# Kernel tuning notes

Measured on AMD Instinct MI355X. Metric: run time of the kernel, lower is better.

Reference implementation:

```python
import jax, jax.numpy as jnp
import numpy as np
from jax import lax

REPR_IN = (32, 16, 8)   # multiplicities of l=0,1,2 fields
SIZE = 5                # cubic kernel size (odd)
PAD = SIZE // 2


def setup_inputs() -> dict:
    key = jax.random.key(0)
    k1, k2 = jax.random.split(key)
    c_in = sum(mul * (2 * l + 1) for l, mul in enumerate(REPR_IN))   # 120
    n_non_scalar = sum(REPR_IN[1:])                                   # 24
    x = jax.random.normal(k1, (2, c_in, 48, 48, 48), dtype=jnp.float32)
    # SE3Convolution materialized as its effective dense conv kernel [O, I, D, H, W]
    fan_in = c_in * SIZE ** 3
    w_gate = jax.random.normal(k2, (n_non_scalar, c_in, SIZE, SIZE, SIZE), dtype=jnp.float32) / np.sqrt(fan_in)
    return {"x": x, "w_gate": w_gate}


def reference(x, w_gate):
    B, _, X, Y, Z = x.shape
    # Gate branch: 3D conv (same padding) -> sigmoid, one scalar gate per non-scalar field
    g = jax.nn.sigmoid(
        lax.conv_general_dilated(
            x, w_gate,
            window_strides=(1, 1, 1),
            padding=[(PAD, PAD)] * 3,
            dimension_numbers=("NCDHW", "OIDHW", "NCDHW"),
        )
    )  # [B, n_non_scalar, X, Y, Z]

    parts = []
    begin_x = 0
    begin_g = 0
    for l, mul in enumerate(REPR_IN):
        if mul == 0:
            continue
        dim = 2 * l + 1
        field_x = x[:, begin_x:begin_x + mul * dim]
        if l == 0:
            # scalar activation on the l=0 block
            parts.append(jax.nn.relu(field_x))
        else:
            # broadcast gate over the 2l+1 components of each field copy
            fx = field_x.reshape(B, mul, dim, X, Y, Z)
            fg = g[:, begin_g:begin_g + mul][:, :, None]      # [B, mul, 1, X, Y, Z]
            begin_g += mul
            parts.append((fx * fg).reshape(B, mul * dim, X, Y, Z))
        begin_x += mul * dim
    return jnp.concatenate(parts, axis=1)
```

## Files before the change

### kernel.cpp

```cpp
#include <hip/hip_runtime.h>

typedef __attribute__((ext_vector_type(8))) short short8;
typedef __attribute__((ext_vector_type(4))) float f32x4;

#define SDIM 48
#define SS   (48*48)
#define SSS  (48*48*48)
#define CIN  120
#define CIP  128
#define NCO  24
#define ZP   52
#define NTAP 125

#define WP_USHORTS (4*25*5*32*32)
#define WP_BYTES   ((size_t)WP_USHORTS*2)
#define XT_USHORTS ((size_t)2*48*48*ZP*CIP)
#define XT_BYTES   (XT_USHORTS*2)
#define WTOT_F32   (NCO*CIN*NTAP)

#define A_CHUNKS 1664
#define ABUF_USH 13312
#define GLP      25

__device__ __forceinline__ unsigned short f2bf(float f){
    unsigned u = __float_as_uint(f);
    u = (u + 0x7FFFu + ((u >> 16) & 1u)) >> 16;
    return (unsigned short)u;
}

__device__ __forceinline__ void gload_lds16(const unsigned short* g, unsigned short* l)
{
    __builtin_amdgcn_global_load_lds(
        (const __attribute__((address_space(1))) unsigned int*)g,
        (__attribute__((address_space(3))) unsigned int*)l,
        16, 0, 0);
}


__global__ __launch_bounds__(256)
void transpose_x(const float* __restrict__ x, unsigned short* __restrict__ xt)
{
    __shared__ unsigned short sm[CIN*50];
    int bid = blockIdx.x;
    const int iy = bid % 48; bid /= 48;
    const int ix = bid % 48;
    const int b  = bid / 48;
    const int tid = threadIdx.x;

    const float* __restrict__ src = x + (size_t)b*CIN*SSS + ((size_t)ix*48 + iy)*48;
    for (int idx = tid; idx < CIN*48; idx += 256) {
        int ci = idx / 48, z = idx - ci*48;
        sm[ci*50 + z] = f2bf(src[(size_t)ci*SSS + z]);
    }
    __syncthreads();
    unsigned short* __restrict__ dst = xt + (((size_t)(b*48 + ix)*48) + iy)*ZP*CIP;
    for (int odx = tid; odx < ZP*CIP; odx += 256) {
        int zp = odx >> 7, ci = odx & 127;
        int z = zp - 2;
        unsigned short v = 0;
        if (ci < CIN && (unsigned)z < 48u) v = sm[ci*50 + z];
        dst[odx] = v;
    }
}

__global__ __launch_bounds__(256)
void repack_w_bf16(const float* __restrict__ w, unsigned short* __restrict__ wp)
{
    int idx = blockIdx.x*256 + threadIdx.x;
    if (idx >= WP_USHORTS) return;
    int cik = idx & 31;
    int co  = (idx >> 5) & 31;
    int dz  = (idx >> 10) % 5;
    int t   = (idx / 5120) % 25;
    int cc  = idx / 128000;
    int ci  = cc*32 + cik;
    float v = 0.f;
    if (co < NCO && ci < CIN)
        v = w[(size_t)(co*CIN + ci)*NTAP + t*5 + dz];
    wp[idx] = f2bf(v);
}

#define MFMA16(a,b,c) __builtin_amdgcn_mfma_f32_16x16x32_bf16(a,b,c,0,0,0)

__global__ __launch_bounds__(128, 3)
void conv_mfma(const unsigned short* __restrict__ xt,
               const unsigned short* __restrict__ wp,
               const float* __restrict__ x,
               float* __restrict__ out)
{
    __shared__ __align__(16) unsigned short As[ABUF_USH];

    int bid = (blockIdx.x & 7) * 144 + (blockIdx.x >> 3);
    const int oyq = bid % 12; bid /= 12;
    const int ox = bid % 48;
    const int b  = bid / 48;

    const int tid = threadIdx.x;
    const int wave = tid >> 6, lane = tid & 63;
    const int l15 = lane & 15, l4 = lane >> 4;
    const int iy0 = oyq*4 - 2;

    const int dxlo = (ox < 2) ? (2 - ox) : 0;
    const int dxhi = (ox > 45) ? (49 - ox) : 4;
    const int ndx  = dxhi - dxlo + 1;

    int goff[13];
    bool ok[13];
#pragma unroll
    for (int k = 0; k < 13; ++k) {
        int L = k*128 + tid;
        int iyl = L / 208, r = L - iyl*208;
        int zp = r >> 2, sf = r & 3;
        int sg = sf ^ ((zp >> 1) & 3);
        int iy = iy0 + iyl;
        ok[k]   = (unsigned)iy < 48u;
        goff[k] = (iy*52 + zp)*128 + sg*8;
    }
    const unsigned short* zsrc = xt + (lane & 31)*8;

    f32x4 acc[2][3][2];
#pragma unroll
    for (int oh = 0; oh < 2; ++oh)
#pragma unroll
      for (int zb = 0; zb < 3; ++zb)
#pragma unroll
        for (int nt = 0; nt < 2; ++nt) acc[oh][zb][nt] = (f32x4){0,0,0,0};

#pragma unroll 1
    for (int cc = 0; cc < 4; ++cc) {
#pragma unroll 1
      for (int dxi = 0; dxi < ndx; ++dxi) {
        const int dx = dxlo + dxi;
        const int ix = ox + dx - 2;
        const unsigned short* __restrict__ slab =
            xt + (size_t)(b*48 + ix)*(48*52*128) + cc*32;

        __syncthreads();
#pragma unroll
        for (int k = 0; k < 13; ++k) {
            const unsigned short* src = ok[k] ? (slab + goff[k]) : zsrc;
            gload_lds16(src, As + k*1024 + wave*512);
        }
        asm volatile("s_waitcnt vmcnt(0)" ::: "memory");
        __builtin_amdgcn_sched_barrier(0);
        __syncthreads();

        const unsigned short* __restrict__ wdxb =
            wp + (size_t)cc*128000 + (size_t)dx*25600 + l15*32 + l4*8;
        const char* __restrict__ asb = (const char*)As;
#pragma unroll
        for (int dz = 0; dz < 5; ++dz) {
            short8 bb[5][2];
#pragma unroll
            for (int dy = 0; dy < 5; ++dy) {
                bb[dy][0] = *(const short8*)(wdxb + dy*5120 + dz*1024);
                bb[dy][1] = *(const short8*)(wdxb + dy*5120 + dz*1024 + 512);
            }
#pragma unroll
            for (int r = 0; r < 6; ++r) {
                const char* __restrict__ ab = asb + (wave*2 + r)*3328;
                short8 a[3];
#pragma unroll
                for (int zb = 0; zb < 3; ++zb) {
                    const int zp = l15 + dz + zb*16;
                    const int off = zp*64 + ((l4 ^ ((zp >> 1) & 3)) << 4);
                    a[zb] = *(const short8*)(ab + off);
                }
                if (r <= 4) {
#pragma unroll
                    for (int zb = 0; zb < 3; ++zb) {
                        acc[0][zb][0] = MFMA16(a[zb], bb[r][0], acc[0][zb][0]);
                        acc[0][zb][1] = MFMA16(a[zb], bb[r][1], acc[0][zb][1]);
                    }
                }
                if (r >= 1) {
#pragma unroll
                    for (int zb = 0; zb < 3; ++zb) {
                        acc[1][zb][0] = MFMA16(a[zb], bb[r-1][0], acc[1][zb][0]);
                        acc[1][zb][1] = MFMA16(a[zb], bb[r-1][1], acc[1][zb][1]);
                    }
                }
            }
        }
      }
    }

    __syncthreads();
    float* gl = (float*)As;

#pragma unroll
    for (int nt = 0; nt < 2; ++nt) {
        const int co = nt*16 + l15;
        if (co < NCO) {
#pragma unroll
            for (int oh = 0; oh < 2; ++oh)
#pragma unroll
              for (int zb = 0; zb < 3; ++zb)
#pragma unroll
                for (int r = 0; r < 4; ++r) {
                    const int z0 = zb*16 + l4*4 + r;
                    gl[((wave*2 + oh)*48 + z0)*GLP + co] =
                        1.f / (1.f + __expf(-acc[oh][zb][nt][r]));
                }
        }
    }
    __syncthreads();

    for (int i = tid; i < 384; i += 128) {
        const int pnt = i % 192;
        const int half = i / 192;
        const int z = pnt % 48, oyl = pnt / 48;
        const int oy2 = oyq*4 + oyl;
        const size_t sp = ((size_t)ox*48 + oy2)*48 + z;
        const float* __restrict__ xsp = x   + (size_t)b*CIN*SSS + sp;
        float*       __restrict__ osp = out + (size_t)b*CIN*SSS + sp;
        const float* __restrict__ gp = gl + pnt*GLP;
        for (int c = half*60; c < half*60 + 60; ++c) {
            float v = xsp[(size_t)c*SSS];
            float o;
            if (c < 32)       o = v > 0.f ? v : 0.f;
            else if (c < 80)  o = v * gp[(c - 32) / 3];
            else              o = v * gp[16 + (c - 80) / 5];
            osp[(size_t)c*SSS] = o;
        }
    }
}


__global__ __launch_bounds__(256)
void repack_w_f32(const float* __restrict__ w, float* __restrict__ wpf)
{
    int idx = blockIdx.x * 256 + threadIdx.x;
    if (idx >= WTOT_F32) return;
    int co = idx % NCO;
    int t  = idx / NCO;
    wpf[idx] = w[co * (CIN * NTAP) + t];
}

__global__ __launch_bounds__(128)
void gated_act_f32(const float* __restrict__ x,
                   const float* __restrict__ wpf,
                   float* __restrict__ out)
{
    const int gid = blockIdx.x * 128 + threadIdx.x;
    const int oz = gid % SDIM;
    int r = gid / SDIM;
    const int oy = r % SDIM; r /= SDIM;
    const int ox = r % SDIM;
    const int b  = r / SDIM;

    const float* __restrict__ xb = x + (size_t)b * CIN * SSS;
    float acc[NCO];
#pragma unroll
    for (int i = 0; i < NCO; ++i) acc[i] = 0.f;

    int izc[5]; bool okz[5];
#pragma unroll
    for (int dz = 0; dz < 5; ++dz) {
        int iz = oz + dz - 2;
        okz[dz] = (unsigned)iz < (unsigned)SDIM;
        izc[dz] = okz[dz] ? iz : 0;
    }
    for (int ci = 0; ci < CIN; ++ci) {
        const float* __restrict__ xc = xb + (size_t)ci * SSS;
        const float* __restrict__ wc = wpf + ci * (NTAP * NCO);
#pragma unroll 1
        for (int dx = 0; dx < 5; ++dx) {
            const int ix = ox + dx - 2;
            const bool okx = (unsigned)ix < (unsigned)SDIM;
            const int ixc = okx ? ix : 0;
#pragma unroll 1
            for (int dy = 0; dy < 5; ++dy) {
                const int iy = oy + dy - 2;
                const bool oky = (unsigned)iy < (unsigned)SDIM;
                const int iyc = oky ? iy : 0;
                const bool okxy = okx && oky;
                const float* __restrict__ xrow = xc + ixc * SS + iyc * SDIM;
                float xv[5];
#pragma unroll
                for (int dz = 0; dz < 5; ++dz) {
                    float v = xrow[izc[dz]];
                    xv[dz] = (okxy && okz[dz]) ? v : 0.f;
                }
                const float* __restrict__ wr = wc + (dx * 25 + dy * 5) * NCO;
#pragma unroll
                for (int dz = 0; dz < 5; ++dz) {
                    const float v = xv[dz];
#pragma unroll
                    for (int co = 0; co < NCO; ++co)
                        acc[co] = fmaf(v, wr[dz * NCO + co], acc[co]);
                }
            }
        }
    }
    float g[NCO];
#pragma unroll
    for (int co = 0; co < NCO; ++co)
        g[co] = 1.f / (1.f + __expf(-acc[co]));

    const size_t sbase = (size_t)b * CIN * SSS + ox * SS + oy * SDIM + oz;
    float* __restrict__ ob = out + sbase;
    const float* __restrict__ xs = x + sbase;
#pragma unroll
    for (int c = 0; c < 32; ++c) {
        float v = xs[(size_t)c * SSS];
        ob[(size_t)c * SSS] = v > 0.f ? v : 0.f;
    }
#pragma unroll
    for (int m = 0; m < 16; ++m) {
        const float gv = g[m];
#pragma unroll
        for (int k = 0; k < 3; ++k) {
            const int c = 32 + m * 3 + k;
            ob[(size_t)c * SSS] = xs[(size_t)c * SSS] * gv;
        }
    }
#pragma unroll
    for (int m = 0; m < 8; ++m) {
        const float gv = g[16 + m];
#pragma unroll
        for (int k = 0; k < 5; ++k) {
            const int c = 80 + m * 5 + k;
            ob[(size_t)c * SSS] = xs[(size_t)c * SSS] * gv;
        }
    }
}

extern "C" void kernel_launch(void* const* d_in, const int* in_sizes, int n_in,
                              void* d_out, int out_size, void* d_ws, size_t ws_size,
                              hipStream_t stream)
{
    const float* x = (const float*)d_in[0];
    const float* w = (const float*)d_in[1];
    float* out = (float*)d_out;

    if (ws_size >= WP_BYTES + XT_BYTES) {
        unsigned short* wp  = (unsigned short*)d_ws;
        unsigned short* xtb = (unsigned short*)((char*)d_ws + WP_BYTES);
        hipLaunchKernelGGL(repack_w_bf16, dim3((WP_USHORTS + 255) / 256), dim3(256),
                           0, stream, w, wp);
        hipLaunchKernelGGL(transpose_x, dim3(2*48*48), dim3(256), 0, stream, x, xtb);
        hipLaunchKernelGGL(conv_mfma, dim3(2*48*12), dim3(128), 0, stream,
                           xtb, wp, x, out);
    } else if (ws_size >= (size_t)WTOT_F32 * 4) {
        float* wpf = (float*)d_ws;
        hipLaunchKernelGGL(repack_w_f32, dim3((WTOT_F32 + 255) / 256), dim3(256),
                           0, stream, w, wpf);
        hipLaunchKernelGGL(gated_act_f32, dim3(2*SSS/128), dim3(128), 0, stream,
                           x, wpf, out);
    }
}
```

Measured before the change: 319.9 us.

## Double-buffer LDS input slabs and prefetch next slab during MFMA loop

Doubles the LDS A buffer and preloads the first slab before the loop. Inside each dz step it issues async global-to-LDS loads for the next (cc,dx) slab, so load latency overlaps with the MFMA work and one barrier per iteration goes away. It also groups LDS reads for two rows ahead of their MFMAs and raises wave priority around the compute. LDS use doubles to about 53KB per block, which may cut occupancy below the launch-bounds target of 3 blocks.

```diff
diff --git a/kernel.cpp b/kernel.cpp
--- a/kernel.cpp
+++ b/kernel.cpp
@@ -88,7 +88,7 @@
                const float* __restrict__ x,
                float* __restrict__ out)
 {
-    __shared__ __align__(16) unsigned short As[ABUF_USH];
+    __shared__ __align__(16) unsigned short As[2*ABUF_USH];
 
     int bid = (blockIdx.x & 7) * 144 + (blockIdx.x >> 3);
     const int oyq = bid % 12; bid /= 12;
@@ -109,10 +109,10 @@
 #pragma unroll
     for (int k = 0; k < 13; ++k) {
         int L = k*128 + tid;
-        int iyl = L / 208, r = L - iyl*208;
-        int zp = r >> 2, sf = r & 3;
+        int row = L / 208, rem = L - row*208;
+        int zp = rem >> 2, sf = rem & 3;
         int sg = sf ^ ((zp >> 1) & 3);
-        int iy = iy0 + iyl;
+        int iy = iy0 + row;
         ok[k]   = (unsigned)iy < 48u;
         goff[k] = (iy*52 + zp)*128 + sg*8;
     }
@@ -126,66 +126,101 @@
 #pragma unroll
         for (int nt = 0; nt < 2; ++nt) acc[oh][zb][nt] = (f32x4){0,0,0,0};
 
+    {
+        const unsigned short* __restrict__ slab =
+            xt + (size_t)(b*48 + ox + dxlo - 2)*(48*52*128);
+#pragma unroll
+        for (int k = 0; k < 13; ++k) {
+            const unsigned short* src = ok[k] ? (slab + goff[k]) : zsrc;
+            gload_lds16(src, As + k*1024 + wave*512);
+        }
+    }
+    asm volatile("s_waitcnt vmcnt(0)" ::: "memory");
+    __builtin_amdgcn_sched_barrier(0);
+    __syncthreads();
+
+    int pcur = 0;
 #pragma unroll 1
     for (int cc = 0; cc < 4; ++cc) {
 #pragma unroll 1
       for (int dxi = 0; dxi < ndx; ++dxi) {
         const int dx = dxlo + dxi;
-        const int ix = ox + dx - 2;
-        const unsigned short* __restrict__ slab =
-            xt + (size_t)(b*48 + ix)*(48*52*128) + cc*32;
-
-        __syncthreads();
-#pragma unroll
-        for (int k = 0; k < 13; ++k) {
-            const unsigned short* src = ok[k] ? (slab + goff[k]) : zsrc;
-            gload_lds16(src, As + k*1024 + wave*512);
-        }
-        asm volatile("s_waitcnt vmcnt(0)" ::: "memory");
-        __builtin_amdgcn_sched_barrier(0);
-        __syncthreads();
+        unsigned short* __restrict__ curb = As + pcur*ABUF_USH;
+        unsigned short* __restrict__ nxtb = As + (pcur^1)*ABUF_USH;
+
+        const int more = (dxi + 1 < ndx);
+        const int cc2 = more ? cc : cc + 1;
+        const int dx2 = more ? dx + 1 : dxlo;
+        const bool do_stage = (cc2 < 4);
+        const unsigned short* __restrict__ slab2 =
+            xt + (size_t)(b*48 + ox + dx2 - 2)*(48*52*128) + cc2*32;
 
         const unsigned short* __restrict__ wdxb =
             wp + (size_t)cc*128000 + (size_t)dx*25600 + l15*32 + l4*8;
-        const char* __restrict__ asb = (const char*)As;
+        const char* __restrict__ asb = (const char*)curb;
+
 #pragma unroll
         for (int dz = 0; dz < 5; ++dz) {
+            if (do_stage) {
+                const int g0 = (dz < 3) ? dz*3 : 9 + (dz - 3)*2;
+                const int gn = (dz < 3) ? 3 : 2;
+#pragma unroll
+                for (int j = 0; j < gn; ++j) {
+                    const int k = g0 + j;
+                    const unsigned short* src = ok[k] ? (slab2 + goff[k]) : zsrc;
+                    gload_lds16(src, nxtb + k*1024 + wave*512);
+                }
+            }
             short8 bb[5][2];
 #pragma unroll
             for (int dy = 0; dy < 5; ++dy) {
                 bb[dy][0] = *(const short8*)(wdxb + dy*5120 + dz*1024);
                 bb[dy][1] = *(const short8*)(wdxb + dy*5120 + dz*1024 + 512);
             }
-#pragma unroll
-            for (int r = 0; r < 6; ++r) {
-                const char* __restrict__ ab = asb + (wave*2 + r)*3328;
-                short8 a[3];
-#pragma unroll
-                for (int zb = 0; zb < 3; ++zb) {
-                    const int zp = l15 + dz + zb*16;
-                    const int off = zp*64 + ((l4 ^ ((zp >> 1) & 3)) << 4);
-                    a[zb] = *(const short8*)(ab + off);
-                }
-                if (r <= 4) {
+            __builtin_amdgcn_s_setprio(1);
+#pragma unroll
+            for (int rp = 0; rp < 3; ++rp) {
+                short8 a[2][3];
+#pragma unroll
+                for (int ri = 0; ri < 2; ++ri) {
+                    const int r = rp*2 + ri;
+                    const char* __restrict__ ab = asb + (wave*2 + r)*3328;
 #pragma unroll
                     for (int zb = 0; zb < 3; ++zb) {
-                        acc[0][zb][0] = MFMA16(a[zb], bb[r][0], acc[0][zb][0]);
-                        acc[0][zb][1] = MFMA16(a[zb], bb[r][1], acc[0][zb][1]);
+                        const int zp = l15 + dz + zb*16;
+                        const int off = zp*64 + ((l4 ^ ((zp >> 1) & 3)) << 4);
+                        a[ri][zb] = *(const short8*)(ab + off);
                     }
                 }
-                if (r >= 1) {
-#pragma unroll
-                    for (int zb = 0; zb < 3; ++zb) {
-                        acc[1][zb][0] = MFMA16(a[zb], bb[r-1][0], acc[1][zb][0]);
-                        acc[1][zb][1] = MFMA16(a[zb], bb[r-1][1], acc[1][zb][1]);
+#pragma unroll
+                for (int ri = 0; ri < 2; ++ri) {
+                    const int r = rp*2 + ri;
+                    if (r <= 4) {
+#pragma unroll
+                        for (int zb = 0; zb < 3; ++zb) {
+                            acc[0][zb][0] = MFMA16(a[ri][zb], bb[r][0], acc[0][zb][0]);
+                            acc[0][zb][1] = MFMA16(a[ri][zb], bb[r][1], acc[0][zb][1]);
+                        }
                     }
+                    if (r >= 1) {
+#pragma unroll
+                        for (int zb = 0; zb < 3; ++zb) {
+                            acc[1][zb][0] = MFMA16(a[ri][zb], bb[r-1][0], acc[1][zb][0]);
+                            acc[1][zb][1] = MFMA16(a[ri][zb], bb[r-1][1], acc[1][zb][1]);
+                        }
+                    }
                 }
             }
-        }
+            __builtin_amdgcn_s_setprio(0);
+        }
+
+        asm volatile("s_waitcnt vmcnt(0)" ::: "memory");
+        __builtin_amdgcn_sched_barrier(0);
+        __syncthreads();
+        pcur ^= 1;
       }
     }
 
-    __syncthreads();
     float* gl = (float*)As;
 
 #pragma unroll
```

Measured after the change: 392.5 us. 1.23x slower.

## Prefetch next input slab into registers while computing current slab

Applied to the files above, without the earlier changes.

Replaces the direct global-to-LDS loads, which waited on vmcnt(0) before every compute step, with register staging. The next (cc,dx) slab is loaded into registers before the MFMA loop over the current one and written to LDS afterwards between two barriers. This hides global load latency behind compute. The cost is 13 extra 16-byte registers per thread, so launch bounds drop from 3 to 2 blocks per SIMD, and MFMA sections get raised wave priority via s_setprio.

```diff
diff --git a/kernel.cpp b/kernel.cpp
--- a/kernel.cpp
+++ b/kernel.cpp
@@ -1,6 +1,7 @@
 #include <hip/hip_runtime.h>
 
 typedef __attribute__((ext_vector_type(8))) short short8;
+typedef __attribute__((ext_vector_type(8))) unsigned short ushort8;
 typedef __attribute__((ext_vector_type(4))) float f32x4;
 
 #define SDIM 48
@@ -26,14 +27,6 @@
     unsigned u = __float_as_uint(f);
     u = (u + 0x7FFFu + ((u >> 16) & 1u)) >> 16;
     return (unsigned short)u;
-}
-
-__device__ __forceinline__ void gload_lds16(const unsigned short* g, unsigned short* l)
-{
-    __builtin_amdgcn_global_load_lds(
-        (const __attribute__((address_space(1))) unsigned int*)g,
-        (__attribute__((address_space(3))) unsigned int*)l,
-        16, 0, 0);
 }
 
 
@@ -82,7 +75,7 @@
 
 #define MFMA16(a,b,c) __builtin_amdgcn_mfma_f32_16x16x32_bf16(a,b,c,0,0,0)
 
-__global__ __launch_bounds__(128, 3)
+__global__ __launch_bounds__(128, 2)
 void conv_mfma(const unsigned short* __restrict__ xt,
                const unsigned short* __restrict__ wp,
                const float* __restrict__ x,
@@ -96,7 +89,8 @@
     const int b  = bid / 48;
 
     const int tid = threadIdx.x;
-    const int wave = tid >> 6, lane = tid & 63;
+    const int lane = tid & 63;
+    const int wave = tid >> 6;
     const int l15 = lane & 15, l4 = lane >> 4;
     const int iy0 = oyq*4 - 2;
 
@@ -109,14 +103,14 @@
 #pragma unroll
     for (int k = 0; k < 13; ++k) {
         int L = k*128 + tid;
-        int iyl = L / 208, r = L - iyl*208;
-        int zp = r >> 2, sf = r & 3;
+        int row = L / 208, rem = L - row*208;
+        int zp = rem >> 2, sf = rem & 3;
         int sg = sf ^ ((zp >> 1) & 3);
-        int iy = iy0 + iyl;
+        int iy = iy0 + row;
         ok[k]   = (unsigned)iy < 48u;
         goff[k] = (iy*52 + zp)*128 + sg*8;
     }
-    const unsigned short* zsrc = xt + (lane & 31)*8;
+    const ushort8 zv = {0,0,0,0,0,0,0,0};
 
     f32x4 acc[2][3][2];
 #pragma unroll
@@ -125,25 +119,38 @@
       for (int zb = 0; zb < 3; ++zb)
 #pragma unroll
         for (int nt = 0; nt < 2; ++nt) acc[oh][zb][nt] = (f32x4){0,0,0,0};
+
+    ushort8 stg[13];
+
+    {
+        const unsigned short* __restrict__ slab =
+            xt + (size_t)(b*48 + ox + dxlo - 2)*(48*52*128);
+#pragma unroll
+        for (int k = 0; k < 13; ++k)
+            stg[k] = ok[k] ? *(const ushort8*)(slab + goff[k]) : zv;
+#pragma unroll
+        for (int k = 0; k < 13; ++k)
+            *(ushort8*)(As + k*1024 + tid*8) = stg[k];
+    }
+    __syncthreads();
 
 #pragma unroll 1
     for (int cc = 0; cc < 4; ++cc) {
 #pragma unroll 1
       for (int dxi = 0; dxi < ndx; ++dxi) {
         const int dx = dxlo + dxi;
-        const int ix = ox + dx - 2;
-        const unsigned short* __restrict__ slab =
-            xt + (size_t)(b*48 + ix)*(48*52*128) + cc*32;
-
-        __syncthreads();
-#pragma unroll
-        for (int k = 0; k < 13; ++k) {
-            const unsigned short* src = ok[k] ? (slab + goff[k]) : zsrc;
-            gload_lds16(src, As + k*1024 + wave*512);
-        }
-        asm volatile("s_waitcnt vmcnt(0)" ::: "memory");
-        __builtin_amdgcn_sched_barrier(0);
-        __syncthreads();
+
+        const int more = (dxi + 1 < ndx);
+        const int cc2 = more ? cc : cc + 1;
+        const int dx2 = more ? dx + 1 : dxlo;
+        const bool do_stage = (cc2 < 4);
+        if (do_stage) {
+            const unsigned short* __restrict__ slab2 =
+                xt + (size_t)(b*48 + ox + dx2 - 2)*(48*52*128) + cc2*32;
+#pragma unroll
+            for (int k = 0; k < 13; ++k)
+                stg[k] = ok[k] ? *(const ushort8*)(slab2 + goff[k]) : zv;
+        }
 
         const unsigned short* __restrict__ wdxb =
             wp + (size_t)cc*128000 + (size_t)dx*25600 + l15*32 + l4*8;
@@ -156,6 +163,7 @@
                 bb[dy][0] = *(const short8*)(wdxb + dy*5120 + dz*1024);
                 bb[dy][1] = *(const short8*)(wdxb + dy*5120 + dz*1024 + 512);
             }
+            __builtin_amdgcn_s_setprio(1);
 #pragma unroll
             for (int r = 0; r < 6; ++r) {
                 const char* __restrict__ ab = asb + (wave*2 + r)*3328;
@@ -181,11 +189,19 @@
                     }
                 }
             }
-        }
+            __builtin_amdgcn_s_setprio(0);
+        }
+
+        __syncthreads();
+        if (do_stage) {
+#pragma unroll
+            for (int k = 0; k < 13; ++k)
+                *(ushort8*)(As + k*1024 + tid*8) = stg[k];
+        }
+        __syncthreads();
       }
     }
 
-    __syncthreads();
     float* gl = (float*)As;
 
 #pragma unroll
```

Result: slower. 363.6 us (+13.7%).
